# Kernel tuning notes

Hardware: AMD Instinct MI355X
Metric: run time of the kernel (lower is better)

## Reference

```python
import jax, jax.numpy as jnp
import numpy as np
from jax import lax

B, N, S, NS = 32, 2048, 256, 16   # batch, seeds, proposals (must be 16*16), ball-query samples
C_IN = 256                         # seed_feat_dim
RADIUS = 0.3
EPS = 1e-5
NAB, NVP = 12, 12                  # num_angle_bin, num_viewpoint
GROUPS, PLANES = 4, 64             # SpatialCGNL groups / bottleneck planes
C_OUT = 2 + 3 + 1 + 1 + 2 * NAB + NVP  # 43


def fps(xyz, npoint):
    """Furthest point sampling (torch pointnet2 style: start at index 0)."""
    Bb, Nn, _ = xyz.shape
    def step(carry, _):
        dist, far = carry
        cen = jnp.take_along_axis(xyz, far[:, None, None], axis=1)      # (B,1,3)
        d = jnp.sum((xyz - cen) ** 2, axis=-1)                          # (B,N)
        dist = jnp.minimum(dist, d)
        return (dist, jnp.argmax(dist, axis=1).astype(jnp.int32)), far
    init = (jnp.full((Bb, Nn), 1e10, xyz.dtype), jnp.zeros((Bb,), jnp.int32))
    _, inds = lax.scan(step, init, None, length=npoint)
    return jnp.transpose(inds)  # (B,npoint)


def ball_query(xyz, new_xyz, radius, nsample):
    """First-nsample neighbors within radius; pad by duplicating the first hit."""
    d2 = jnp.sum((new_xyz[:, :, None, :] - xyz[:, None, :, :]) ** 2, axis=-1)  # (B,S,N)
    Nn = xyz.shape[1]
    cand = jnp.where(d2 < radius * radius, jnp.arange(Nn)[None, None, :], Nn)
    idx = jnp.sort(cand, axis=-1)[..., :nsample]
    idx = jnp.where(idx == Nn, idx[..., :1], idx)   # duplicate first hit
    idx = jnp.where(idx == Nn, 0, idx)              # no neighbor at all -> 0
    return idx


def bn1d(x, g, b, m, v):
    """Inference BatchNorm1d over channel axis of (B,C,S)."""
    s = (g * lax.rsqrt(v + EPS))
    return (x - m[None, :, None]) * s[None, :, None] + b[None, :, None]


def forward(xyz, features, sa_w0, sa_w1, sa_w2, sa_gamma, sa_beta, sa_mean, sa_var,
            wt, wp, wg, wz, gn_gamma, gn_beta,
            c1_w, c1_b, bn1_g, bn1_b, bn1_m, bn1_v,
            c2_w, c2_b, bn2_g, bn2_b, bn2_m, bn2_v, c3_w, c3_b):
    # ---- PointnetSAModuleVotes (vote_fps sampling) ----
    fps_inds = fps(xyz, S)                                               # (B,S)
    new_xyz = jnp.take_along_axis(xyz, fps_inds[:, :, None], axis=1)     # (B,S,3)
    idx = ball_query(xyz, new_xyz, RADIUS, NS)                           # (B,S,NS)
    gather = jax.vmap(lambda a, i: a[i])
    g_xyz = (gather(xyz, idx) - new_xyz[:, :, None, :]) / RADIUS         # (B,S,NS,3), normalize_xyz
    g_feat = gather(jnp.transpose(features, (0, 2, 1)), idx)             # (B,S,NS,C)
    h = jnp.concatenate([g_xyz, g_feat], axis=-1)                        # (B,S,NS,3+C)
    for i, w in enumerate((sa_w0, sa_w1, sa_w2)):                        # SharedMLP: conv1x1(no bias)+BN+ReLU
        h = jnp.einsum('bsnc,oc->bsno', h, w)
        h = jax.nn.relu((h - sa_mean[i]) * (sa_gamma[i] * lax.rsqrt(sa_var[i] + EPS)) + sa_beta[i])
    x = jnp.transpose(jnp.max(h, axis=2), (0, 2, 1))                     # max-pool over NS -> (B,128,S)

    # ---- SpatialCGNL (use_scale=False, groups=4), spatial 16x16 flattened to S ----
    t = jnp.einsum('oc,bcn->bon', wt, x)                                 # (B,64,S)
    p = jnp.einsum('oc,bcn->bon', wp, x)
    g = jnp.einsum('oc,bcn->bon', wg, x)
    cg = PLANES // GROUPS                                                # 16
    tg = t.reshape(B, GROUPS, cg * S)
    pg = p.reshape(B, GROUPS, cg * S)
    gg = g.reshape(B, GROUPS, cg * S)
    att = jnp.sum(pg * gg, axis=-1, keepdims=True)                       # (B,G,1) scalar per group
    y = (att * tg).reshape(B, GROUPS, cg, S)                             # (B,G,16,S)
    wz_g = wz.reshape(GROUPS, 128 // GROUPS, cg)                         # grouped 1x1 conv 64->128
    y = jnp.einsum('goc,bgcn->bgon', wz_g, y).reshape(B, 128, S)
    # GroupNorm(num_groups=4, num_channels=128)
    yg = y.reshape(B, GROUPS, -1)
    mu = jnp.mean(yg, axis=-1, keepdims=True)
    var = jnp.mean((yg - mu) ** 2, axis=-1, keepdims=True)
    yn = ((yg - mu) * lax.rsqrt(var + EPS)).reshape(B, 128, S)
    y = yn * gn_gamma[None, :, None] + gn_beta[None, :, None] + x        # affine + residual

    # ---- conv/bn/relu head ----
    h1 = jax.nn.relu(bn1d(jnp.einsum('oc,bcn->bon', c1_w, y) + c1_b[None, :, None], bn1_g, bn1_b, bn1_m, bn1_v))
    h2 = jax.nn.relu(bn1d(jnp.einsum('oc,bcn->bon', c2_w, h1) + c2_b[None, :, None], bn2_g, bn2_b, bn2_m, bn2_v))
    net = jnp.einsum('oc,bcn->bon', c3_w, h2) + c3_b[None, :, None]      # (B,43,S)

    # ---- decode_scores ----
    nt = jnp.transpose(net, (0, 2, 1))                                   # (B,S,43)
    center = new_xyz + nt[:, :, 2:5]
    ang_res_n = nt[:, :, 7 + NAB:7 + 2 * NAB]
    out = jnp.concatenate([
        nt[:, :, 0:2],                    # objectness_scores
        center,                           # center
        nt[:, :, 5:7 + 2 * NAB],          # width, quality, angle_scores, angle_residuals_normalized
        ang_res_n * jnp.float32(np.pi / NAB),  # angle_residuals
        nt[:, :, 7 + 2 * NAB:],           # viewpoint_scores
    ], axis=-1)                           # (B,S,55)
    return out


def setup_inputs():
    key = jax.random.key(0)
    ks = iter(jax.random.split(key, 32))
    rn = lambda shape, s=0.05: jax.random.normal(next(ks), shape, jnp.float32) * s
    return dict(
        xyz=rn((B, N, 3), 1.0),
        features=rn((B, C_IN, N), 1.0),
        sa_w0=rn((128, C_IN + 3)), sa_w1=rn((128, 128)), sa_w2=rn((128, 128)),
        sa_gamma=jnp.ones((3, 128)), sa_beta=jnp.zeros((3, 128)),
        sa_mean=jnp.zeros((3, 128)), sa_var=jnp.ones((3, 128)),
        wt=rn((PLANES, 128)), wp=rn((PLANES, 128)), wg=rn((PLANES, 128)),
        wz=rn((128, PLANES // GROUPS)),
        gn_gamma=jnp.ones((128,)), gn_beta=jnp.zeros((128,)),
        c1_w=rn((128, 128)), c1_b=jnp.zeros((128,)),
        bn1_g=jnp.ones((128,)), bn1_b=jnp.zeros((128,)), bn1_m=jnp.zeros((128,)), bn1_v=jnp.ones((128,)),
        c2_w=rn((128, 128)), c2_b=jnp.zeros((128,)),
        bn2_g=jnp.ones((128,)), bn2_b=jnp.zeros((128,)), bn2_m=jnp.zeros((128,)), bn2_v=jnp.ones((128,)),
        c3_w=rn((C_OUT, 128)), c3_b=jnp.zeros((C_OUT,)),
    )


def reference(xyz, features, sa_w0, sa_w1, sa_w2, sa_gamma, sa_beta, sa_mean, sa_var,
              wt, wp, wg, wz, gn_gamma, gn_beta,
              c1_w, c1_b, bn1_g, bn1_b, bn1_m, bn1_v,
              c2_w, c2_b, bn2_g, bn2_b, bn2_m, bn2_v, c3_w, c3_b):
    return forward(xyz, features, sa_w0, sa_w1, sa_w2, sa_gamma, sa_beta, sa_mean, sa_var,
                   wt, wp, wg, wz, gn_gamma, gn_beta,
                   c1_w, c1_b, bn1_g, bn1_b, bn1_m, bn1_v,
                   c2_w, c2_b, bn2_g, bn2_b, bn2_m, bn2_v, c3_w, c3_b)
```

## Files before the change

kernel.cpp:

```cpp
#include <hip/hip_runtime.h>
#include <hip/hip_bf16.h>
#include <math.h>

#define Bx   32
#define Nx   2048
#define Sx   256
#define NSx  16
#define CINx 256

typedef unsigned short u16;
typedef unsigned int   u32;
typedef unsigned long long u64;
typedef short bf16x8 __attribute__((ext_vector_type(8)));
typedef float f32x4  __attribute__((ext_vector_type(4)));
typedef float f32x16 __attribute__((ext_vector_type(16)));

__device__ __forceinline__ float b2f(u16 u) {
  union { u32 i; float f; } v; v.i = ((u32)u) << 16; return v.f;
}
__device__ __forceinline__ u16 f2b(float x) {
  u32 u = __float_as_uint(x);
  u32 r = (u + 0x7FFFu + ((u >> 16) & 1u)) >> 16;
  return (u16)r;
}
__device__ __forceinline__ float ldin(const void* p, size_t i, int bf) {
  return bf ? b2f(((const u16*)p)[i]) : ((const float*)p)[i];
}

#define DPP_FMAX(x, ctrl)                                                      \
  x = fmaxf(x, __int_as_float(__builtin_amdgcn_update_dpp(                     \
          __float_as_int(x), __float_as_int(x), (ctrl), 0xf, 0xf, false)))

#define OFF_FEATT 0
#define OFF_XT    (33554432)
#define OFF_T     (OFF_XT + 4194304)
#define OFF_YT    (OFF_T + 2097152)
#define OFF_NXYZ  (OFF_YT + 4194304)
#define OFF_IDX   (OFF_NXYZ + 98304)
#define OFF_ATT   (OFF_IDX + 524288)
#define OFF_W0F   (OFF_ATT + 512)
#define OFF_B0    (OFF_W0F + 133120)
#define OFF_W1F   (OFF_B0 + 512)
#define OFF_B1    (OFF_W1F + 65536)
#define OFF_W2F   (OFF_B1 + 512)
#define OFF_B2    (OFF_W2F + 65536)
#define OFF_WTT   (OFF_B2 + 512)
#define OFF_WPT   (OFF_WTT + 32768)
#define OFF_WGT   (OFF_WPT + 32768)
#define OFF_C1T   (OFF_WGT + 32768)
#define OFF_D1    (OFF_C1T + 65536)
#define OFF_C2T   (OFF_D1 + 512)
#define OFF_D2    (OFF_C2T + 65536)
#define OFF_C3T   (OFF_D2 + 512)
#define OFF_WZF   (OFF_C3T + 22016)
#define OFF_GNG   (OFF_WZF + 8192)
#define OFF_GNB   (OFF_GNG + 512)
#define OFF_C3B   (OFF_GNB + 512)
#define OFF_FLAG  (OFF_C3B + 512)

__global__ __launch_bounds__(256) void k_sniff(const u32* __restrict__ w, int* __restrict__ flag) {
  __shared__ int cnt;
  int t = threadIdx.x;
  if (t == 0) cnt = 0;
  __syncthreads();
  u32 x = w[t];
  int e_lo = (x >> 7) & 0xFF;
  if (e_lo >= 100 && e_lo <= 140) atomicAdd(&cnt, 1);
  __syncthreads();
  if (t == 0) *flag = (cnt > 128) ? 1 : 0;
}

#define TRANS_BLKS 4096
__global__ __launch_bounds__(256) void k_mega(
    const void* __restrict__ xyzR, const void* __restrict__ featR,
    const void* sa_w0, const void* sa_w1, const void* sa_w2,
    const void* sa_g,  const void* sa_b,  const void* sa_m, const void* sa_v,
    const void* wt, const void* wp, const void* wg, const void* wzI,
    const void* gngI, const void* gnbI,
    const void* c1w, const void* c1b,
    const void* bn1g, const void* bn1b, const void* bn1m, const void* bn1v,
    const void* c2w, const void* c2b,
    const void* bn2g, const void* bn2b, const void* bn2m, const void* bn2v,
    const void* c3w, const void* c3bI,
    float* __restrict__ nxyz, u16* __restrict__ featT,
    u16* __restrict__ w0F, float* __restrict__ b0, u16* __restrict__ w1F, float* __restrict__ b1,
    u16* __restrict__ w2F, float* __restrict__ b2,
    float* __restrict__ wtT, float* __restrict__ wpT, float* __restrict__ wgT,
    float* __restrict__ c1T, float* __restrict__ d1, float* __restrict__ c2T, float* __restrict__ d2,
    float* __restrict__ c3T, float* __restrict__ wzF, float* __restrict__ gngF,
    float* __restrict__ gnbF, float* __restrict__ c3bF,
    const int* __restrict__ flagp) {
  __shared__ union {
    struct { float sxyz[Nx * 3]; u64 red[2][4]; } fps;
    u16 tile[64][65];
  } sm;
  int bid = blockIdx.x, t = threadIdx.x;
  int bf = *flagp;

  if (bid < Bx) {
    int b = bid;
    const size_t xb = (size_t)b * Nx * 3;
    for (int i = t; i < Nx * 3; i += 256) sm.fps.sxyz[i] = ldin(xyzR, xb + i, bf);
    __syncthreads();
    float px[8], py[8], pz[8], dist[8];
#pragma unroll
    for (int j = 0; j < 8; ++j) {
      int p = t * 8 + j;
      px[j] = sm.fps.sxyz[p * 3 + 0];
      py[j] = sm.fps.sxyz[p * 3 + 1];
      pz[j] = sm.fps.sxyz[p * 3 + 2];
      dist[j] = 1e10f;
    }
    int lane = t & 63, w = t >> 6;
    int far = 0, myind = 0;
    for (int it = 0; it < Sx; ++it) {
      if (t == it) myind = far;
      float cx = sm.fps.sxyz[far * 3 + 0];
      float cy = sm.fps.sxyz[far * 3 + 1];
      float cz = sm.fps.sxyz[far * 3 + 2];
      float bv = -1.f; int bj = 0;
#pragma unroll
      for (int j = 0; j < 8; ++j) {
        float dx = __fsub_rn(px[j], cx);
        float dy = __fsub_rn(py[j], cy);
        float dz = __fsub_rn(pz[j], cz);
        float d = __fadd_rn(__fadd_rn(__fmul_rn(dx, dx), __fmul_rn(dy, dy)), __fmul_rn(dz, dz));
        float nd = fminf(dist[j], d);
        dist[j] = nd;
        if (nd > bv) { bv = nd; bj = j; }
      }
      int bi = t * 8 + bj;
      float x = bv;
      DPP_FMAX(x, 0x111);
      DPP_FMAX(x, 0x112);
      DPP_FMAX(x, 0x114);
      DPP_FMAX(x, 0x118);
      DPP_FMAX(x, 0x142);
      DPP_FMAX(x, 0x143);
      float wmax = __int_as_float(__builtin_amdgcn_readlane(__float_as_int(x), 63));
      u64 mk = __ballot(bv == wmax);
      int srcl = (int)__builtin_ctzll(mk);
      int wbi = __builtin_amdgcn_readlane(bi, srcl);
      if (lane == 63)
        sm.fps.red[it & 1][w] = ((u64)__float_as_uint(wmax) << 32) | (u32)(~wbi);
      __syncthreads();
      u64 k0 = sm.fps.red[it & 1][0], k1 = sm.fps.red[it & 1][1];
      u64 k2 = sm.fps.red[it & 1][2], k3 = sm.fps.red[it & 1][3];
      u64 best = k0 > k1 ? k0 : k1;
      if (k2 > best) best = k2;
      if (k3 > best) best = k3;
      far = (int)(u32)(~(u32)best);
    }
    float* o = nxyz + ((size_t)b * Sx + t) * 3;
    o[0] = sm.fps.sxyz[myind * 3 + 0];
    o[1] = sm.fps.sxyz[myind * 3 + 1];
    o[2] = sm.fps.sxyz[myind * 3 + 2];
  } else if (bid < Bx + TRANS_BLKS) {
    int tb = bid - Bx;
    int nblk = tb & 31, rest = tb >> 5;
    int cblk = rest & 3, b = rest >> 2;
    int n0 = nblk * 64, c0 = cblk * 64;
    int tx = t & 63, ty = t >> 6;
#pragma unroll
    for (int r = ty; r < 64; r += 4) {
      size_t src = ((size_t)(b * CINx + c0 + r)) * Nx + n0 + tx;
      sm.tile[r][tx] = bf ? ((const u16*)featR)[src] : f2b(((const float*)featR)[src]);
    }
    __syncthreads();
#pragma unroll
    for (int r = ty; r < 64; r += 4)
      featT[((size_t)(b * Nx + n0 + r)) * CINx + c0 + tx] = sm.tile[tx][r];
  } else {
    int g0 = (bid - Bx - TRANS_BLKS) * 256 + t;
    const int gs = 64 * 256;
    for (int i = g0; i < 18 * 4 * 64 * 8; i += gs) {
      int j = i & 7, lane = (i >> 3) & 63, nt = (i >> 9) & 3, kt = i >> 11;
      int o = nt * 32 + (lane & 31);
      int c = kt * 16 + ((lane >> 5) << 3) + j;
      float s = ldin(sa_g, o, bf) * rsqrtf(ldin(sa_v, o, bf) + 1e-5f);
      float w;
      if (c < 256) w = ldin(sa_w0, o * 259 + 3 + c, bf);
      else if (c < 259) w = ldin(sa_w0, o * 259 + (c - 256), bf);
      else w = 0.f;
      w0F[i] = f2b(w * s);
    }
    for (int i = g0; i < 8 * 4 * 64 * 8; i += gs) {
      int j = i & 7, lane = (i >> 3) & 63, nt = (i >> 9) & 3, kt = i >> 11;
      int o = nt * 32 + (lane & 31);
      int c = kt * 16 + ((lane >> 5) << 3) + j;
      float s1 = ldin(sa_g, 128 + o, bf) * rsqrtf(ldin(sa_v, 128 + o, bf) + 1e-5f);
      float s2 = ldin(sa_g, 256 + o, bf) * rsqrtf(ldin(sa_v, 256 + o, bf) + 1e-5f);
      w1F[i] = f2b(ldin(sa_w1, o * 128 + c, bf) * s1);
      w2F[i] = f2b(ldin(sa_w2, o * 128 + c, bf) * s2);
    }
    for (int o = g0; o < 128; o += gs) {
      float s0 = ldin(sa_g, o, bf)       * rsqrtf(ldin(sa_v, o, bf)       + 1e-5f);
      float s1 = ldin(sa_g, 128 + o, bf) * rsqrtf(ldin(sa_v, 128 + o, bf) + 1e-5f);
      float s2 = ldin(sa_g, 256 + o, bf) * rsqrtf(ldin(sa_v, 256 + o, bf) + 1e-5f);
      b0[o] = ldin(sa_b, o, bf)       - ldin(sa_m, o, bf)       * s0;
      b1[o] = ldin(sa_b, 128 + o, bf) - ldin(sa_m, 128 + o, bf) * s1;
      b2[o] = ldin(sa_b, 256 + o, bf) - ldin(sa_m, 256 + o, bf) * s2;
      float sc1 = ldin(bn1g, o, bf) * rsqrtf(ldin(bn1v, o, bf) + 1e-5f);
      float sc2 = ldin(bn2g, o, bf) * rsqrtf(ldin(bn2v, o, bf) + 1e-5f);
      d1[o] = (ldin(c1b, o, bf) - ldin(bn1m, o, bf)) * sc1 + ldin(bn1b, o, bf);
      d2[o] = (ldin(c2b, o, bf) - ldin(bn2m, o, bf)) * sc2 + ldin(bn2b, o, bf);
      gngF[o] = ldin(gngI, o, bf);
      gnbF[o] = ldin(gnbI, o, bf);
    }
    for (int i = g0; i < 128 * 128; i += gs) {
      int o = i >> 7, c = i & 127;
      float sc1 = ldin(bn1g, o, bf) * rsqrtf(ldin(bn1v, o, bf) + 1e-5f);
      float sc2 = ldin(bn2g, o, bf) * rsqrtf(ldin(bn2v, o, bf) + 1e-5f);
      c1T[c * 128 + o] = ldin(c1w, i, bf) * sc1;
      c2T[c * 128 + o] = ldin(c2w, i, bf) * sc2;
    }
    for (int i = g0; i < 64 * 128; i += gs) {
      int o = i >> 7, c = i & 127;
      wtT[c * 64 + o] = ldin(wt, i, bf);
      wpT[c * 64 + o] = ldin(wp, i, bf);
      wgT[c * 64 + o] = ldin(wg, i, bf);
    }
    for (int i = g0; i < 43 * 128; i += gs) {
      int o = i >> 7, c = i & 127;
      c3T[c * 43 + o] = ldin(c3w, i, bf);
    }
    for (int i = g0; i < 2048; i += gs) wzF[i] = ldin(wzI, i, bf);
    for (int i = g0; i < 43; i += gs) c3bF[i] = ldin(c3bI, i, bf);
  }
}

__global__ __launch_bounds__(256) void k_ballq(const void* __restrict__ xyzR,
                                               const float* __restrict__ nxyz,
                                               int* __restrict__ idxb,
                                               const int* __restrict__ flagp) {
  int bf = *flagp;
  int t = threadIdx.x;
  int wv = t >> 6, lane = t & 63;
  int gs = blockIdx.x * 4 + wv;
  int b = gs >> 8;
  const size_t xb = (size_t)b * Nx * 3;
  const float* cen = nxyz + (size_t)gs * 3;
  float cx = cen[0], cy = cen[1], cz = cen[2];
  const float R2 = (float)(0.3 * 0.3);
  int* outp = idxb + (size_t)gs * NSx;
  int have = 0, first = 0;
  bool gotfirst = false;
  for (int ch = 0; ch < Nx / 64 && have < NSx; ++ch) {
    int p = ch * 64 + lane;
    float dx = __fsub_rn(ldin(xyzR, xb + p * 3 + 0, bf), cx);
    float dy = __fsub_rn(ldin(xyzR, xb + p * 3 + 1, bf), cy);
    float dz = __fsub_rn(ldin(xyzR, xb + p * 3 + 2, bf), cz);
    float d2 = __fadd_rn(__fadd_rn(__fmul_rn(dx, dx), __fmul_rn(dy, dy)), __fmul_rn(dz, dz));
    bool hit = d2 < R2;
    unsigned long long m = __ballot(hit);
    if (hit) {
      int pos = have + __popcll(m & ((1ull << lane) - 1ull));
      if (pos < NSx) outp[pos] = p;
    }
    if (!gotfirst && m) { first = ch * 64 + (int)__builtin_ctzll(m); gotfirst = true; }
    have += __popcll(m);
  }
  if (have < NSx && lane >= have && lane < NSx) outp[lane] = first;
}

__global__ __launch_bounds__(256) void k_samlp(
    const u16* __restrict__ featT, const void* __restrict__ xyzR,
    const float* __restrict__ nxyz, const int* __restrict__ idxb,
    const u16* __restrict__ w0F, const float* __restrict__ b0v,
    const u16* __restrict__ w1F, const float* __restrict__ b1v,
    const u16* __restrict__ w2F, const float* __restrict__ b2v,
    float* __restrict__ xT, const int* __restrict__ flagp) {
  __shared__ __align__(16) u16 lds[4][32 * 32 + 2 * 32 * 136];
  int bf = *flagp;
  int t = threadIdx.x, w = t >> 6, lane = t & 63;
  int b = blockIdx.y;
  int s0 = (blockIdx.x * 4 + w) * 2;
  u16* ht = &lds[w][0];
  u16* hA = &lds[w][1024];
  u16* hB = &lds[w][1024 + 4352];
  int m = lane & 31, half = lane >> 5;
  const int* gidx = idxb + ((size_t)b * Sx + s0) * NSx;
  int pn = gidx[m];
  for (int i = lane; i < 32 * 32; i += 64)
    if ((i & 31) >= 3) ht[i] = 0;
  for (int i = lane; i < 96; i += 64) {
    int mm = i / 3, cc = i - (i / 3) * 3;
    int pn2 = gidx[mm];
    float cen = nxyz[((size_t)b * Sx + s0 + (mm >> 4)) * 3 + cc];
    float v = (ldin(xyzR, ((size_t)b * Nx + pn2) * 3 + cc, bf) - cen) * (1.0f / 0.3f);
    ht[mm * 32 + cc] = f2b(v);
  }
  __syncthreads();

  const bf16x8* wf0 = (const bf16x8*)w0F;
  const bf16x8* wf1 = (const bf16x8*)w1F;
  const bf16x8* wf2 = (const bf16x8*)w2F;
  f32x16 acc[4];

#pragma unroll
  for (int nt = 0; nt < 4; ++nt) acc[nt] = (f32x16)(0.f);
  const u16* arow = featT + ((size_t)b * Nx + pn) * CINx + half * 8;
#pragma unroll
  for (int kt = 0; kt < 18; ++kt) {
    bf16x8 a = (kt < 16) ? *(const bf16x8*)(arow + kt * 16)
                         : *(const bf16x8*)(ht + m * 32 + (kt - 16) * 16 + half * 8);
#pragma unroll
    for (int nt = 0; nt < 4; ++nt)
      acc[nt] = __builtin_amdgcn_mfma_f32_32x32x16_bf16(a, wf0[(kt * 4 + nt) * 64 + lane], acc[nt], 0, 0, 0);
  }
#pragma unroll
  for (int nt = 0; nt < 4; ++nt) {
    float bb = b0v[nt * 32 + m];
#pragma unroll
    for (int r = 0; r < 16; ++r) {
      int mm = (r & 3) + 8 * (r >> 2) + 4 * half;
      hA[mm * 136 + nt * 32 + m] = f2b(fmaxf(acc[nt][r] + bb, 0.f));
    }
  }
  __syncthreads();

#pragma unroll
  for (int nt = 0; nt < 4; ++nt) acc[nt] = (f32x16)(0.f);
#pragma unroll
  for (int kt = 0; kt < 8; ++kt) {
    bf16x8 a = *(const bf16x8*)(hA + m * 136 + kt * 16 + half * 8);
#pragma unroll
    for (int nt = 0; nt < 4; ++nt)
      acc[nt] = __builtin_amdgcn_mfma_f32_32x32x16_bf16(a, wf1[(kt * 4 + nt) * 64 + lane], acc[nt], 0, 0, 0);
  }
#pragma unroll
  for (int nt = 0; nt < 4; ++nt) {
    float bb = b1v[nt * 32 + m];
#pragma unroll
    for (int r = 0; r < 16; ++r) {
      int mm = (r & 3) + 8 * (r >> 2) + 4 * half;
      hB[mm * 136 + nt * 32 + m] = f2b(fmaxf(acc[nt][r] + bb, 0.f));
    }
  }
  __syncthreads();

#pragma unroll
  for (int nt = 0; nt < 4; ++nt) acc[nt] = (f32x16)(0.f);
#pragma unroll
  for (int kt = 0; kt < 8; ++kt) {
    bf16x8 a = *(const bf16x8*)(hB + m * 136 + kt * 16 + half * 8);
#pragma unroll
    for (int nt = 0; nt < 4; ++nt)
      acc[nt] = __builtin_amdgcn_mfma_f32_32x32x16_bf16(a, wf2[(kt * 4 + nt) * 64 + lane], acc[nt], 0, 0, 0);
  }
#pragma unroll
  for (int nt = 0; nt < 4; ++nt) {
    float v0 = acc[nt][0], v1 = acc[nt][8];
#pragma unroll
    for (int r = 1; r < 8; ++r) { v0 = fmaxf(v0, acc[nt][r]); v1 = fmaxf(v1, acc[nt][8 + r]); }
    v0 = fmaxf(v0, __shfl_xor(v0, 32, 64));
    v1 = fmaxf(v1, __shfl_xor(v1, 32, 64));
    int o = nt * 32 + m;
    float vv = half ? v1 : v0;
    xT[((size_t)b * Sx + s0 + half) * 128 + o] = fmaxf(vv + b2v[o], 0.f);
  }
}

__device__ __forceinline__ float blocksum(float v, volatile float* red, int t) {
#pragma unroll
  for (int off = 32; off; off >>= 1) v += __shfl_down(v, off, 64);
  __syncthreads();
  if ((t & 63) == 0) red[t >> 6] = v;
  __syncthreads();
  return red[0] + red[1] + red[2] + red[3];
}

__global__ __launch_bounds__(256) void k_tpgn(const float* __restrict__ xT,
                                              const float* __restrict__ wtT,
                                              const float* __restrict__ wpT,
                                              const float* __restrict__ wgT,
                                              const float* __restrict__ wzF,
                                              const float* __restrict__ gngF,
                                              const float* __restrict__ gnbF,
                                              float* __restrict__ yT) {
  __shared__ float xs[64][129];
  __shared__ float tS[16][260];
  __shared__ float wzs[32][16];
  __shared__ float red[4];
  int g = blockIdx.x, b = blockIdx.y, t = threadIdx.x;
  for (int i = t; i < 512; i += 256)
    wzs[i >> 4][i & 15] = wzF[(g * 32 + (i >> 4)) * 16 + (i & 15)];
  int r = t >> 4, sg = t & 15;
  float attp = 0.f;
  for (int tile = 0; tile < 4; ++tile) {
    {
      int rr = t >> 2, part = (t & 3) * 32;
      const float4* src = (const float4*)(xT + ((size_t)b * Sx + tile * 64 + rr) * 128 + part);
#pragma unroll
      for (int q = 0; q < 8; ++q) {
        float4 v = src[q];
        xs[rr][part + q * 4 + 0] = v.x;
        xs[rr][part + q * 4 + 1] = v.y;
        xs[rr][part + q * 4 + 2] = v.z;
        xs[rr][part + q * 4 + 3] = v.w;
      }
    }
    __syncthreads();
    float ta[4], pa[4], ga[4];
#pragma unroll
    for (int j = 0; j < 4; ++j) { ta[j] = 0.f; pa[j] = 0.f; ga[j] = 0.f; }
    for (int c = 0; c < 128; ++c) {
      float wa = wtT[c * 64 + g * 16 + r];
      float wb = wpT[c * 64 + g * 16 + r];
      float wc = wgT[c * 64 + g * 16 + r];
#pragma unroll
      for (int j = 0; j < 4; ++j) {
        float xv = xs[sg * 4 + j][c];
        ta[j] = fmaf(wa, xv, ta[j]);
        pa[j] = fmaf(wb, xv, pa[j]);
        ga[j] = fmaf(wc, xv, ga[j]);
      }
    }
#pragma unroll
    for (int j = 0; j < 4; ++j) {
      attp += pa[j] * ga[j];
      tS[r][tile * 64 + sg * 4 + j] = ta[j];
    }
    __syncthreads();
  }
  float attv = blocksum(attp, red, t);
  int s = t;
  float yv[32];
#pragma unroll
  for (int o = 0; o < 32; ++o) yv[o] = 0.f;
  for (int c = 0; c < 16; ++c) {
    float tv = attv * tS[c][s];
#pragma unroll
    for (int o = 0; o < 32; ++o) yv[o] = fmaf(wzs[o][c], tv, yv[o]);
  }
  float ls = 0.f;
#pragma unroll
  for (int o = 0; o < 32; ++o) ls += yv[o];
  float mu = blocksum(ls, red, t) * (1.f / 8192.f);
  float lq = 0.f;
#pragma unroll
  for (int o = 0; o < 32; ++o) { float d = yv[o] - mu; lq = fmaf(d, d, lq); }
  float var = blocksum(lq, red, t) * (1.f / 8192.f);
  float rs = rsqrtf(var + 1e-5f);
  const float* xrow = xT + ((size_t)b * Sx + s) * 128 + g * 32;
  float* yrow = yT + ((size_t)b * Sx + s) * 128 + g * 32;
#pragma unroll
  for (int o = 0; o < 32; ++o) {
    int ch = g * 32 + o;
    yrow[o] = (yv[o] - mu) * rs * gngF[ch] + gnbF[ch] + xrow[o];
  }
}

__global__ __launch_bounds__(256) void k_ffn(const float* __restrict__ yT,
                                             const float* __restrict__ c1T, const float* __restrict__ d1,
                                             const float* __restrict__ c2T, const float* __restrict__ d2,
                                             const float* __restrict__ c3T, const float* __restrict__ c3bF,
                                             const float* __restrict__ nxyz,
                                             void* __restrict__ outp,
                                             const int* __restrict__ flagp) {
  __shared__ float ys[32][132];
  __shared__ float h1s[32][132];
  __shared__ float h2s[32][132];
  __shared__ float nets[32][44];
  int bf = *flagp;
  int b = blockIdx.y, s0 = blockIdx.x * 32, t = threadIdx.x;
  {
    int r = t >> 3, part = (t & 7) * 16;
    const float4* src = (const float4*)(yT + ((size_t)b * Sx + s0 + r) * 128 + part);
#pragma unroll
    for (int q = 0; q < 4; ++q) *(float4*)&ys[r][part + q * 4] = src[q];
  }
  __syncthreads();
  int o0 = (t & 31) * 4, sl0 = (t >> 5) * 4;
  float acc[16];
#pragma unroll
  for (int k = 0; k < 16; ++k) acc[k] = 0.f;
  for (int c = 0; c < 128; ++c) {
    float4 wv = *(const float4*)(c1T + c * 128 + o0);
    float yv[4];
#pragma unroll
    for (int j = 0; j < 4; ++j) yv[j] = ys[sl0 + j][c];
#pragma unroll
    for (int j = 0; j < 4; ++j) {
      acc[0 * 4 + j] = fmaf(wv.x, yv[j], acc[0 * 4 + j]);
      acc[1 * 4 + j] = fmaf(wv.y, yv[j], acc[1 * 4 + j]);
      acc[2 * 4 + j] = fmaf(wv.z, yv[j], acc[2 * 4 + j]);
      acc[3 * 4 + j] = fmaf(wv.w, yv[j], acc[3 * 4 + j]);
    }
  }
  {
    float4 dv = *(const float4*)(d1 + o0);
    float db[4] = {dv.x, dv.y, dv.z, dv.w};
#pragma unroll
    for (int i = 0; i < 4; ++i)
#pragma unroll
      for (int j = 0; j < 4; ++j)
        h1s[sl0 + j][o0 + i] = fmaxf(acc[i * 4 + j] + db[i], 0.f);
  }
  __syncthreads();
#pragma unroll
  for (int k = 0; k < 16; ++k) acc[k] = 0.f;
  for (int c = 0; c < 128; ++c) {
    float4 wv = *(const float4*)(c2T + c * 128 + o0);
    float yv[4];
#pragma unroll
    for (int j = 0; j < 4; ++j) yv[j] = h1s[sl0 + j][c];
#pragma unroll
    for (int j = 0; j < 4; ++j) {
      acc[0 * 4 + j] = fmaf(wv.x, yv[j], acc[0 * 4 + j]);
      acc[1 * 4 + j] = fmaf(wv.y, yv[j], acc[1 * 4 + j]);
      acc[2 * 4 + j] = fmaf(wv.z, yv[j], acc[2 * 4 + j]);
      acc[3 * 4 + j] = fmaf(wv.w, yv[j], acc[3 * 4 + j]);
    }
  }
  {
    float4 dv = *(const float4*)(d2 + o0);
    float db[4] = {dv.x, dv.y, dv.z, dv.w};
#pragma unroll
    for (int i = 0; i < 4; ++i)
#pragma unroll
      for (int j = 0; j < 4; ++j)
        h2s[sl0 + j][o0 + i] = fmaxf(acc[i * 4 + j] + db[i], 0.f);
  }
  __syncthreads();
  for (int f = t; f < 43 * 32; f += 256) {
    int o = f >> 5, s = f & 31;
    float a = c3bF[o];
    for (int c4 = 0; c4 < 32; ++c4) {
      float4 hv = *(const float4*)&h2s[s][c4 * 4];
      a = fmaf(hv.x, c3T[(c4 * 4 + 0) * 43 + o], a);
      a = fmaf(hv.y, c3T[(c4 * 4 + 1) * 43 + o], a);
      a = fmaf(hv.z, c3T[(c4 * 4 + 2) * 43 + o], a);
      a = fmaf(hv.w, c3T[(c4 * 4 + 3) * 43 + o], a);
    }
    nets[s][o] = a;
  }
  __syncthreads();
  const float PI12 = (float)(M_PI / 12.0);
  for (int f = t; f < 55 * 32; f += 256) {
    int s = f / 55, kk = f - s * 55;
    float v;
    if (kk < 5) {
      v = nets[s][kk];
      if (kk >= 2) v += nxyz[((size_t)b * Sx + s0 + s) * 3 + (kk - 2)];
    } else if (kk < 31) v = nets[s][kk];
    else if (kk < 43) v = nets[s][kk - 12] * PI12;
    else v = nets[s][kk - 12];
    size_t oi = ((size_t)b * Sx + s0 + s) * 55 + kk;
    if (bf) ((u16*)outp)[oi] = f2b(v);
    else    ((float*)outp)[oi] = v;
  }
}

extern "C" void kernel_launch(void* const* d_in, const int* in_sizes, int n_in,
                              void* d_out, int out_size, void* d_ws, size_t ws_size,
                              hipStream_t stream) {
  char* w = (char*)d_ws;
  u16*   featT = (u16*)(w + OFF_FEATT);
  float* xT    = (float*)(w + OFF_XT);
  float* yT    = (float*)(w + OFF_YT);
  float* nxyz  = (float*)(w + OFF_NXYZ);
  int*   idxb  = (int*)(w + OFF_IDX);
  u16*   w0F   = (u16*)(w + OFF_W0F);
  float* b0    = (float*)(w + OFF_B0);
  u16*   w1F   = (u16*)(w + OFF_W1F);
  float* b1    = (float*)(w + OFF_B1);
  u16*   w2F   = (u16*)(w + OFF_W2F);
  float* b2    = (float*)(w + OFF_B2);
  float* wtT   = (float*)(w + OFF_WTT);
  float* wpT   = (float*)(w + OFF_WPT);
  float* wgT   = (float*)(w + OFF_WGT);
  float* c1T   = (float*)(w + OFF_C1T);
  float* d1    = (float*)(w + OFF_D1);
  float* c2T   = (float*)(w + OFF_C2T);
  float* d2    = (float*)(w + OFF_D2);
  float* c3T   = (float*)(w + OFF_C3T);
  float* wzF   = (float*)(w + OFF_WZF);
  float* gngF  = (float*)(w + OFF_GNG);
  float* gnbF  = (float*)(w + OFF_GNB);
  float* c3bF  = (float*)(w + OFF_C3B);
  int*   flag  = (int*)(w + OFF_FLAG);

  k_sniff<<<1, 256, 0, stream>>>((const u32*)d_in[0], flag);
  k_mega<<<Bx + TRANS_BLKS + 64, 256, 0, stream>>>(
      d_in[0], d_in[1],
      d_in[2], d_in[3], d_in[4], d_in[5], d_in[6], d_in[7], d_in[8],
      d_in[9], d_in[10], d_in[11], d_in[12], d_in[13], d_in[14],
      d_in[15], d_in[16], d_in[17], d_in[18], d_in[19], d_in[20],
      d_in[21], d_in[22], d_in[23], d_in[24], d_in[25], d_in[26],
      d_in[27], d_in[28],
      nxyz, featT,
      w0F, b0, w1F, b1, w2F, b2, wtT, wpT, wgT,
      c1T, d1, c2T, d2, c3T, wzF, gngF, gnbF, c3bF, flag);
  k_ballq<<<(Bx * Sx) / 4, 256, 0, stream>>>(d_in[0], nxyz, idxb, flag);
  k_samlp<<<dim3(Sx / 8, Bx), 256, 0, stream>>>(featT, d_in[0], nxyz, idxb,
                                                w0F, b0, w1F, b1, w2F, b2, xT, flag);
  k_tpgn<<<dim3(4, Bx), 256, 0, stream>>>(xT, wtT, wpT, wgT, wzF, gngF, gnbF, yT);
  k_ffn<<<dim3(8, Bx), 256, 0, stream>>>(yT, c1T, d1, c2T, d2, c3T, c3bF, nxyz,
                                         d_out, flag);
}
```

Before: 477.7 us.

## Fuse ball query into SA MLP kernel and stage attention weights in LDS

Merges the ball-query kernel into the shared-MLP kernel. Each wave scans all points for its two centroids and writes neighbor indices to LDS, removing a launch and the index buffer round trip. The relative-xyz tail goes straight into registers, which drops one K tile of the first GEMM. hA is reused for both hidden layers and the block-wide syncs are removed, cutting LDS use. The ball-query loop now always scans all 2048 points with no early exit, and k_tpgn caches its wt/wp/wg weight slices in shared memory.

```diff
diff --git a/kernel.cpp b/kernel.cpp
--- a/kernel.cpp
+++ b/kernel.cpp
@@ -173,7 +173,7 @@
   } else {
     int g0 = (bid - Bx - TRANS_BLKS) * 256 + t;
     const int gs = 64 * 256;
-    for (int i = g0; i < 18 * 4 * 64 * 8; i += gs) {
+    for (int i = g0; i < 17 * 4 * 64 * 8; i += gs) {
       int j = i & 7, lane = (i >> 3) & 63, nt = (i >> 9) & 3, kt = i >> 11;
       int o = nt * 32 + (lane & 31);
       int c = kt * 16 + ((lane >> 5) << 3) + j;
@@ -229,68 +229,67 @@
   }
 }
 
-__global__ __launch_bounds__(256) void k_ballq(const void* __restrict__ xyzR,
-                                               const float* __restrict__ nxyz,
-                                               int* __restrict__ idxb,
-                                               const int* __restrict__ flagp) {
-  int bf = *flagp;
-  int t = threadIdx.x;
-  int wv = t >> 6, lane = t & 63;
-  int gs = blockIdx.x * 4 + wv;
-  int b = gs >> 8;
-  const size_t xb = (size_t)b * Nx * 3;
-  const float* cen = nxyz + (size_t)gs * 3;
-  float cx = cen[0], cy = cen[1], cz = cen[2];
-  const float R2 = (float)(0.3 * 0.3);
-  int* outp = idxb + (size_t)gs * NSx;
-  int have = 0, first = 0;
-  bool gotfirst = false;
-  for (int ch = 0; ch < Nx / 64 && have < NSx; ++ch) {
-    int p = ch * 64 + lane;
-    float dx = __fsub_rn(ldin(xyzR, xb + p * 3 + 0, bf), cx);
-    float dy = __fsub_rn(ldin(xyzR, xb + p * 3 + 1, bf), cy);
-    float dz = __fsub_rn(ldin(xyzR, xb + p * 3 + 2, bf), cz);
-    float d2 = __fadd_rn(__fadd_rn(__fmul_rn(dx, dx), __fmul_rn(dy, dy)), __fmul_rn(dz, dz));
-    bool hit = d2 < R2;
-    unsigned long long m = __ballot(hit);
-    if (hit) {
-      int pos = have + __popcll(m & ((1ull << lane) - 1ull));
-      if (pos < NSx) outp[pos] = p;
-    }
-    if (!gotfirst && m) { first = ch * 64 + (int)__builtin_ctzll(m); gotfirst = true; }
-    have += __popcll(m);
-  }
-  if (have < NSx && lane >= have && lane < NSx) outp[lane] = first;
-}
-
-__global__ __launch_bounds__(256) void k_samlp(
+__global__ __launch_bounds__(256) void k_fused(
     const u16* __restrict__ featT, const void* __restrict__ xyzR,
-    const float* __restrict__ nxyz, const int* __restrict__ idxb,
+    const float* __restrict__ nxyz,
     const u16* __restrict__ w0F, const float* __restrict__ b0v,
     const u16* __restrict__ w1F, const float* __restrict__ b1v,
     const u16* __restrict__ w2F, const float* __restrict__ b2v,
     float* __restrict__ xT, const int* __restrict__ flagp) {
-  __shared__ __align__(16) u16 lds[4][32 * 32 + 2 * 32 * 136];
+  __shared__ __align__(16) u16 hAa[4][32 * 136];
+  __shared__ int ids[4][32];
   int bf = *flagp;
   int t = threadIdx.x, w = t >> 6, lane = t & 63;
   int b = blockIdx.y;
   int s0 = (blockIdx.x * 4 + w) * 2;
-  u16* ht = &lds[w][0];
-  u16* hA = &lds[w][1024];
-  u16* hB = &lds[w][1024 + 4352];
+  u16* hA = &hAa[w][0];
   int m = lane & 31, half = lane >> 5;
-  const int* gidx = idxb + ((size_t)b * Sx + s0) * NSx;
-  int pn = gidx[m];
-  for (int i = lane; i < 32 * 32; i += 64)
-    if ((i & 31) >= 3) ht[i] = 0;
-  for (int i = lane; i < 96; i += 64) {
-    int mm = i / 3, cc = i - (i / 3) * 3;
-    int pn2 = gidx[mm];
-    float cen = nxyz[((size_t)b * Sx + s0 + (mm >> 4)) * 3 + cc];
-    float v = (ldin(xyzR, ((size_t)b * Nx + pn2) * 3 + cc, bf) - cen) * (1.0f / 0.3f);
-    ht[mm * 32 + cc] = f2b(v);
-  }
-  __syncthreads();
+  const size_t xb = (size_t)b * Nx * 3;
+
+  const float* cen0 = nxyz + ((size_t)b * Sx + s0) * 3;
+  float c0x = cen0[0], c0y = cen0[1], c0z = cen0[2];
+  float c1x = cen0[3], c1y = cen0[4], c1z = cen0[5];
+
+  const float R2 = (float)(0.3 * 0.3);
+  u64 below = (lane == 63) ? 0x7fffffffffffffffull : ((1ull << lane) - 1ull);
+  int have0 = 0, have1 = 0;
+  for (int ch = 0; ch < Nx / 64; ++ch) {
+    int p = ch * 64 + lane;
+    float px = ldin(xyzR, xb + p * 3 + 0, bf);
+    float py = ldin(xyzR, xb + p * 3 + 1, bf);
+    float pz = ldin(xyzR, xb + p * 3 + 2, bf);
+    float dx0 = __fsub_rn(px, c0x), dy0 = __fsub_rn(py, c0y), dz0 = __fsub_rn(pz, c0z);
+    float d0 = __fadd_rn(__fadd_rn(__fmul_rn(dx0, dx0), __fmul_rn(dy0, dy0)), __fmul_rn(dz0, dz0));
+    float dx1 = __fsub_rn(px, c1x), dy1 = __fsub_rn(py, c1y), dz1 = __fsub_rn(pz, c1z);
+    float d1 = __fadd_rn(__fadd_rn(__fmul_rn(dx1, dx1), __fmul_rn(dy1, dy1)), __fmul_rn(dz1, dz1));
+    bool h0 = d0 < R2, h1 = d1 < R2;
+    u64 m0 = __ballot(h0), m1 = __ballot(h1);
+    if (h0) { int pos = have0 + __popcll(m0 & below); if (pos < NSx) ids[w][pos] = p; }
+    if (h1) { int pos = have1 + __popcll(m1 & below); if (pos < NSx) ids[w][16 + pos] = p; }
+    have0 += __popcll(m0);
+    have1 += __popcll(m1);
+  }
+  if (lane < 32) {
+    int c = lane >> 4, i = lane & 15;
+    int hv = c ? have1 : have0;
+    if (i >= hv && i < NSx) ids[w][c * 16 + i] = ids[w][c * 16];
+  }
+  int pn = ids[w][m];
+
+  float rcx = half ? c1x : c0x, rcy = half ? c1y : c0y, rcz = half ? c1z : c0z;
+  float pcx = (m >> 4) ? c1x : c0x, pcy = (m >> 4) ? c1y : c0y, pcz = (m >> 4) ? c1z : c0z;
+  (void)rcx; (void)rcy; (void)rcz;
+  bf16x8 a_tail = (bf16x8)(short)0;
+  {
+    float gx = ldin(xyzR, xb + (size_t)pn * 3 + 0, bf);
+    float gy = ldin(xyzR, xb + (size_t)pn * 3 + 1, bf);
+    float gz = ldin(xyzR, xb + (size_t)pn * 3 + 2, bf);
+    if (half == 0) {
+      a_tail[0] = (short)f2b((gx - pcx) * (1.0f / 0.3f));
+      a_tail[1] = (short)f2b((gy - pcy) * (1.0f / 0.3f));
+      a_tail[2] = (short)f2b((gz - pcz) * (1.0f / 0.3f));
+    }
+  }
 
   const bf16x8* wf0 = (const bf16x8*)w0F;
   const bf16x8* wf1 = (const bf16x8*)w1F;
@@ -301,9 +300,8 @@
   for (int nt = 0; nt < 4; ++nt) acc[nt] = (f32x16)(0.f);
   const u16* arow = featT + ((size_t)b * Nx + pn) * CINx + half * 8;
 #pragma unroll
-  for (int kt = 0; kt < 18; ++kt) {
-    bf16x8 a = (kt < 16) ? *(const bf16x8*)(arow + kt * 16)
-                         : *(const bf16x8*)(ht + m * 32 + (kt - 16) * 16 + half * 8);
+  for (int kt = 0; kt < 17; ++kt) {
+    bf16x8 a = (kt < 16) ? *(const bf16x8*)(arow + kt * 16) : a_tail;
 #pragma unroll
     for (int nt = 0; nt < 4; ++nt)
       acc[nt] = __builtin_amdgcn_mfma_f32_32x32x16_bf16(a, wf0[(kt * 4 + nt) * 64 + lane], acc[nt], 0, 0, 0);
@@ -317,8 +315,6 @@
       hA[mm * 136 + nt * 32 + m] = f2b(fmaxf(acc[nt][r] + bb, 0.f));
     }
   }
-  __syncthreads();
-
 #pragma unroll
   for (int nt = 0; nt < 4; ++nt) acc[nt] = (f32x16)(0.f);
 #pragma unroll
@@ -334,16 +330,14 @@
 #pragma unroll
     for (int r = 0; r < 16; ++r) {
       int mm = (r & 3) + 8 * (r >> 2) + 4 * half;
-      hB[mm * 136 + nt * 32 + m] = f2b(fmaxf(acc[nt][r] + bb, 0.f));
-    }
-  }
-  __syncthreads();
-
+      hA[mm * 136 + nt * 32 + m] = f2b(fmaxf(acc[nt][r] + bb, 0.f));
+    }
+  }
 #pragma unroll
   for (int nt = 0; nt < 4; ++nt) acc[nt] = (f32x16)(0.f);
 #pragma unroll
   for (int kt = 0; kt < 8; ++kt) {
-    bf16x8 a = *(const bf16x8*)(hB + m * 136 + kt * 16 + half * 8);
+    bf16x8 a = *(const bf16x8*)(hA + m * 136 + kt * 16 + half * 8);
 #pragma unroll
     for (int nt = 0; nt < 4; ++nt)
       acc[nt] = __builtin_amdgcn_mfma_f32_32x32x16_bf16(a, wf2[(kt * 4 + nt) * 64 + lane], acc[nt], 0, 0, 0);
@@ -380,11 +374,18 @@
                                               float* __restrict__ yT) {
   __shared__ float xs[64][129];
   __shared__ float tS[16][260];
+  __shared__ float wts[3][128][16];
   __shared__ float wzs[32][16];
   __shared__ float red[4];
   int g = blockIdx.x, b = blockIdx.y, t = threadIdx.x;
   for (int i = t; i < 512; i += 256)
     wzs[i >> 4][i & 15] = wzF[(g * 32 + (i >> 4)) * 16 + (i & 15)];
+  for (int i = t; i < 128 * 16; i += 256) {
+    int c = i >> 4, r2 = i & 15;
+    wts[0][c][r2] = wtT[c * 64 + g * 16 + r2];
+    wts[1][c][r2] = wpT[c * 64 + g * 16 + r2];
+    wts[2][c][r2] = wgT[c * 64 + g * 16 + r2];
+  }
   int r = t >> 4, sg = t & 15;
   float attp = 0.f;
   for (int tile = 0; tile < 4; ++tile) {
@@ -405,9 +406,9 @@
 #pragma unroll
     for (int j = 0; j < 4; ++j) { ta[j] = 0.f; pa[j] = 0.f; ga[j] = 0.f; }
     for (int c = 0; c < 128; ++c) {
-      float wa = wtT[c * 64 + g * 16 + r];
-      float wb = wpT[c * 64 + g * 16 + r];
-      float wc = wgT[c * 64 + g * 16 + r];
+      float wa = wts[0][c][r];
+      float wb = wts[1][c][r];
+      float wc = wts[2][c][r];
 #pragma unroll
       for (int j = 0; j < 4; ++j) {
         float xv = xs[sg * 4 + j][c];
@@ -560,7 +561,6 @@
   float* xT    = (float*)(w + OFF_XT);
   float* yT    = (float*)(w + OFF_YT);
   float* nxyz  = (float*)(w + OFF_NXYZ);
-  int*   idxb  = (int*)(w + OFF_IDX);
   u16*   w0F   = (u16*)(w + OFF_W0F);
   float* b0    = (float*)(w + OFF_B0);
   u16*   w1F   = (u16*)(w + OFF_W1F);
@@ -592,8 +592,7 @@
       nxyz, featT,
       w0F, b0, w1F, b1, w2F, b2, wtT, wpT, wgT,
       c1T, d1, c2T, d2, c3T, wzF, gngF, gnbF, c3bF, flag);
-  k_ballq<<<(Bx * Sx) / 4, 256, 0, stream>>>(d_in[0], nxyz, idxb, flag);
-  k_samlp<<<dim3(Sx / 8, Bx), 256, 0, stream>>>(featT, d_in[0], nxyz, idxb,
+  k_fused<<<dim3(Sx / 8, Bx), 256, 0, stream>>>(featT, d_in[0], nxyz,
                                                 w0F, b0, w1F, b1, w2F, b2, xT, flag);
   k_tpgn<<<dim3(4, Bx), 256, 0, stream>>>(xT, wtT, wpT, wgT, wzF, gngF, gnbF, yT);
   k_ffn<<<dim3(8, Bx), 256, 0, stream>>>(yT, c1T, d1, c2T, d2, c3T, c3bF, nxyz,
```

Result: faster. 433.9 us (-9.2%).
